# Optimization experiments

Measured on AMD Instinct MI355X. Metric: run time of the kernel, lower is better.

Reference implementation:

```python
import jax, jax.numpy as jnp
import numpy as np
from jax import lax

D_MODEL = 1024
INTER = 1024
N_EXPERTS = 8
TOP_K = 2
ROUTE_SCALE = 1.0
B, S = 2, 4096


def setup_inputs() -> dict:
    key = jax.random.key(0)
    ks = jax.random.split(key, 16)
    sc_d = 1.0 / np.sqrt(D_MODEL)
    sc_f = 1.0 / np.sqrt(INTER)
    inp = {
        "x": jax.random.normal(ks[0], (B, S, D_MODEL), dtype=jnp.float32),
        "gate_w": jax.random.normal(ks[1], (N_EXPERTS, D_MODEL), dtype=jnp.float32) * sc_d,
        # stacked routed-expert SwiGLU params
        "w1": jax.random.normal(ks[2], (N_EXPERTS, D_MODEL, INTER), dtype=jnp.float32) * sc_d,
        "b1": jnp.zeros((N_EXPERTS, INTER), dtype=jnp.float32),
        "w2": jax.random.normal(ks[3], (N_EXPERTS, INTER, D_MODEL), dtype=jnp.float32) * sc_f,
        "b2": jnp.zeros((N_EXPERTS, D_MODEL), dtype=jnp.float32),
        "w3": jax.random.normal(ks[4], (N_EXPERTS, D_MODEL, INTER), dtype=jnp.float32) * sc_d,
        "b3": jnp.zeros((N_EXPERTS, INTER), dtype=jnp.float32),
        # shared expert (dense MLP on all tokens)
        "sw1": jax.random.normal(ks[5], (D_MODEL, INTER), dtype=jnp.float32) * sc_d,
        "sb1": jnp.zeros((INTER,), dtype=jnp.float32),
        "sw2": jax.random.normal(ks[6], (INTER, D_MODEL), dtype=jnp.float32) * sc_f,
        "sb2": jnp.zeros((D_MODEL,), dtype=jnp.float32),
        "sw3": jax.random.normal(ks[7], (D_MODEL, INTER), dtype=jnp.float32) * sc_d,
        "sb3": jnp.zeros((INTER,), dtype=jnp.float32),
    }
    return inp


def reference(x, gate_w, w1, b1, w2, b2, w3, b3, sw1, sb1, sw2, sb2, sw3, sb3):
    Bx, Sx, D = x.shape
    xt = x.reshape(-1, D)  # [T, D]

    # --- Gate: softmax scores, top-k experts (n_groups==1, no bias branch) ---
    scores = jax.nn.softmax((xt @ gate_w.T).astype(jnp.float32), axis=-1)  # [T, E]
    top_vals, top_idx = lax.top_k(scores, TOP_K)  # [T, K]
    weights = (top_vals * ROUTE_SCALE).astype(x.dtype)  # gather of original scores == top_vals

    # combine[t, e] = sum_k weights[t, k] * (top_idx[t, k] == e)
    combine = jnp.sum(
        jax.nn.one_hot(top_idx, N_EXPERTS, dtype=x.dtype) * weights[..., None], axis=1
    )  # [T, E]

    # --- Routed experts: scan over experts, weighted accumulate ---
    def body(acc, p):
        W1, B1, W2, B2, W3, B3, c = p  # c: [T] combine weights for this expert
        h = jax.nn.silu(xt @ W1 + B1) * (xt @ W3 + B3)  # [T, INTER]
        return acc + c[:, None] * (h @ W2 + B2), None

    y, _ = lax.scan(body, jnp.zeros_like(xt), (w1, b1, w2, b2, w3, b3, combine.T))

    # --- Shared expert on all tokens ---
    z = (jax.nn.silu(xt @ sw1 + sb1) * (xt @ sw3 + sb3)) @ sw2 + sb2

    return (y + z).reshape(Bx, Sx, D)
```

## Files before the change

### kernel.cpp

```cpp
#include <hip/hip_runtime.h>
#include <hip/hip_bf16.h>
#include <math.h>

#define D_MODEL 1024
#define INTER   1024
#define NEXP    8
#define T_TOK   8192
#define ROWCAP  17408

typedef short  short8 __attribute__((ext_vector_type(8)));
typedef float  f32x4  __attribute__((ext_vector_type(4)));

__device__ __forceinline__ ushort f2bf(float f) {
    uint u = __float_as_uint(f);
    u += 0x7fffu + ((u >> 16) & 1u);
    return (ushort)(u >> 16);
}
__device__ __forceinline__ float bf2f(ushort u) {
    return __uint_as_float((uint)u << 16);
}
__device__ __forceinline__ uint pk2(float lo, float hi) {
    return (uint)f2bf(lo) | ((uint)f2bf(hi) << 16);
}
__device__ __forceinline__ void gll16(const ushort* g, ushort* l) {
    __builtin_amdgcn_global_load_lds(
        (const __attribute__((address_space(1))) unsigned int*)(g),
        (__attribute__((address_space(3))) unsigned int*)(l), 16, 0, 0);
}

#define IDX64(r, c) ((r) * 64 + (((c) ^ ((r) & 7)) * 8))

__global__ __launch_bounds__(256)
void k_gate(const float* __restrict__ X, const float* __restrict__ GW,
            int* __restrict__ topk_idx, float* __restrict__ topk_w,
            int* __restrict__ cnt, ushort* __restrict__ Xb)
{
    __shared__ int lcnt[NEXP];
    const int t = threadIdx.x;
    if (t < NEXP) lcnt[t] = 0;
    const int lane = t & 63, wv = t >> 6;
    float4 gwr[NEXP][4];
#pragma unroll
    for (int e = 0; e < NEXP; ++e)
#pragma unroll
        for (int i = 0; i < 4; ++i)
            gwr[e][i] = *(const float4*)(GW + e * 1024 + i * 256 + lane * 4);
    __syncthreads();
    const int tok0 = blockIdx.x * 32 + wv * 8;
    const bool b0 = lane & 1, b1 = lane & 2, b2 = lane & 4;
    for (int tt = 0; tt < 8; ++tt) {
        const int tok = tok0 + tt;
        const float* xr = X + (size_t)tok * 1024;
        float4 xv[4];
#pragma unroll
        for (int i = 0; i < 4; ++i) xv[i] = *(const float4*)(xr + i * 256 + lane * 4);
#pragma unroll
        for (int i = 0; i < 4; ++i) {
            uint2 o = { pk2(xv[i].x, xv[i].y), pk2(xv[i].z, xv[i].w) };
            *(uint2*)(Xb + (size_t)tok * 1024 + i * 256 + lane * 4) = o;
        }
        float p[NEXP];
#pragma unroll
        for (int e = 0; e < NEXP; ++e) {
            float s = 0.f;
#pragma unroll
            for (int i = 0; i < 4; ++i)
                s += xv[i].x * gwr[e][i].x + xv[i].y * gwr[e][i].y
                   + xv[i].z * gwr[e][i].z + xv[i].w * gwr[e][i].w;
            p[e] = s;
        }
        float q[4];
#pragma unroll
        for (int j = 0; j < 4; ++j) {
            float send = b0 ? p[j] : p[j + 4];
            float recv = __shfl_xor(send, 1, 64);
            q[j] = (b0 ? p[j + 4] : p[j]) + recv;
        }
        float u2[2];
#pragma unroll
        for (int j = 0; j < 2; ++j) {
            float send = b1 ? q[j] : q[j + 2];
            float recv = __shfl_xor(send, 2, 64);
            u2[j] = (b1 ? q[j + 2] : q[j]) + recv;
        }
        float send = b2 ? u2[0] : u2[1];
        float r = (b2 ? u2[1] : u2[0]) + __shfl_xor(send, 4, 64);
        r += __shfl_xor(r, 8, 64);
        r += __shfl_xor(r, 16, 64);
        r += __shfl_xor(r, 32, 64);
        float sc[NEXP];
#pragma unroll
        for (int e = 0; e < NEXP; ++e)
            sc[e] = __shfl(r, ((e & 1) << 2) | (e & 2) | ((e >> 2) & 1), 64);
        float m = sc[0];
#pragma unroll
        for (int e = 1; e < NEXP; ++e) m = fmaxf(m, sc[e]);
        float ssum = 0.f;
#pragma unroll
        for (int e = 0; e < NEXP; ++e) { sc[e] = __expf(sc[e] - m); ssum += sc[e]; }
        float inv = 1.f / ssum;
#pragma unroll
        for (int e = 0; e < NEXP; ++e) sc[e] *= inv;
        int i0 = 0; float v0 = sc[0];
#pragma unroll
        for (int e = 1; e < NEXP; ++e) if (sc[e] > v0) { v0 = sc[e]; i0 = e; }
        int i1 = -1; float v1 = -1e30f;
#pragma unroll
        for (int e = 0; e < NEXP; ++e) if (e != i0 && sc[e] > v1) { v1 = sc[e]; i1 = e; }
        if (lane == 0) {
            topk_idx[2 * tok]     = i0;
            topk_idx[2 * tok + 1] = i1;
            topk_w[2 * tok]       = v0;
            topk_w[2 * tok + 1]   = v1;
            atomicAdd(&lcnt[i0], 1);
            atomicAdd(&lcnt[i1], 1);
        }
    }
    __syncthreads();
    if (t < NEXP) atomicAdd(&cnt[t], lcnt[t]);
}

__global__ void k_prefix(const int* __restrict__ cnt, int* __restrict__ offs)
{
    if (threadIdx.x == 0 && blockIdx.x == 0) {
        int tot = 0;
        for (int e = 0; e < NEXP; ++e) {
            offs[e] = tot;
            tot += ((cnt[e] + 127) / 128) * 128;
        }
        offs[NEXP] = tot;
    }
}

__global__ void k_scatter(const int* __restrict__ topk_idx, const float* __restrict__ topk_w,
                          const int* __restrict__ offs, int* __restrict__ cnt2,
                          int* __restrict__ rowid, float* __restrict__ rowwt,
                          int* __restrict__ rowslot)
{
    __shared__ int loc[NEXP];
    __shared__ int base[NEXP];
    const int t = threadIdx.x;
    if (t < NEXP) loc[t] = 0;
    __syncthreads();
    const int tok = blockIdx.x * 256 + t;
    const int e0 = topk_idx[2 * tok], e1 = topk_idx[2 * tok + 1];
    const int s0 = atomicAdd(&loc[e0], 1);
    const int s1 = atomicAdd(&loc[e1], 1);
    __syncthreads();
    if (t < NEXP) base[t] = atomicAdd(&cnt2[t], loc[t]);
    __syncthreads();
    int p0 = offs[e0] + base[e0] + s0;
    rowid[p0] = tok; rowwt[p0] = topk_w[2 * tok]; rowslot[p0] = 0;
    int p1 = offs[e1] + base[e1] + s1;
    rowid[p1] = tok; rowwt[p1] = topk_w[2 * tok + 1]; rowslot[p1] = 1;
}

__global__ __launch_bounds__(256)
void k_tw(const float* __restrict__ srcA, ushort* __restrict__ dstA, int nA,
          const float* __restrict__ srcB, ushort* __restrict__ dstB, int nB,
          const float* __restrict__ srcC, ushort* __restrict__ dstC)
{
    __shared__ float tl[64][132];
    int m = blockIdx.y;
    const float* src; ushort* dst;
    if (m < nA)           { src = srcA + ((size_t)m << 20); dst = dstA + ((size_t)m << 20); }
    else if ((m -= nA) < nB) { src = srcB + ((size_t)m << 20); dst = dstB + ((size_t)m << 20); }
    else { m -= nB;       src = srcC + ((size_t)m << 20); dst = dstC + ((size_t)m << 20); }
    const int tile = blockIdx.x;
    const int nb = tile >> 4, kt = tile & 15;
    const int t = threadIdx.x;
    const int c4 = (t & 31) * 4, kr = t >> 5;
#pragma unroll
    for (int i = 0; i < 8; ++i) {
        const int kl = kr + 8 * i;
        float4 v = *(const float4*)(src + (size_t)(kt * 64 + kl) * 1024 + nb * 128 + c4);
        tl[kl][c4 + 0] = v.x; tl[kl][c4 + 1] = v.y;
        tl[kl][c4 + 2] = v.z; tl[kl][c4 + 3] = v.w;
    }
    __syncthreads();
    const int nl = t >> 1, h = t & 1;
    ushort* drow = dst + (size_t)tile * 8192 + nl * 64;
#pragma unroll
    for (int w = 0; w < 4; ++w) {
        const int cimg = h * 4 + w;
        const int cl = cimg ^ (nl & 7);
        float f[8];
#pragma unroll
        for (int j = 0; j < 8; ++j) f[j] = tl[cl * 8 + j][nl];
        uint4 o = { pk2(f[0], f[1]), pk2(f[2], f[3]), pk2(f[4], f[5]), pk2(f[6], f[7]) };
        *(uint4*)(drow + cimg * 8) = o;
    }
}

template <bool ROUTED>
__global__ __launch_bounds__(256, 2)
void k_h(const ushort* __restrict__ Xb,
         const ushort* __restrict__ W1t, const float* __restrict__ B1,
         const ushort* __restrict__ W3t, const float* __restrict__ B3,
         ushort* __restrict__ Hb,
         const int* __restrict__ rowid, const int* __restrict__ offs,
         const int* __restrict__ cnt)
{
    __shared__ __align__(16) ushort As [128 * 64];
    __shared__ __align__(16) ushort B1s[128 * 64];
    __shared__ __align__(16) ushort B3s[128 * 64];
    __shared__ int ridc[128];

    const int bid = blockIdx.y * 8 + blockIdx.x;
    const int swz = (bid & 7) * gridDim.y + (bid >> 3);
    const int nbx  = swz & 7;
    const int nb   = nbx * 128;
    const int row0 = (swz >> 3) * 128;

    int rstart = 0, rcount = T_TOK;
    const ushort* w1 = W1t; const ushort* w3 = W3t;
    if constexpr (ROUTED) {
        const int total = offs[NEXP];
        if (row0 >= total) return;
        int e = 0;
        while (offs[e + 1] <= row0) ++e;
        rstart = offs[e]; rcount = cnt[e];
        w1 += (size_t)e << 20; B1 += e * INTER;
        w3 += (size_t)e << 20; B3 += e * INTER;
    }
    const int t = threadIdx.x;
    const ushort* g1 = w1 + (size_t)(nbx * 16) * 8192 + t * 8;
    const ushort* g3 = w3 + (size_t)(nbx * 16) * 8192 + t * 8;

    if constexpr (ROUTED) {
        if (t < 128) {
            const int rr = row0 + t;
            ridc[t] = ((rr - rstart) < rcount) ? rowid[rr] : 0;
        }
        __syncthreads();
    }
    const int sub = t >> 3, ci = t & 7;
    const ushort* asrc[4];
#pragma unroll
    for (int c = 0; c < 4; ++c) {
        const int r = c * 32 + sub;
        const int tok = ROUTED ? ridc[r] : (row0 + r);
        asrc[c] = Xb + (size_t)tok * 1024 + (size_t)((ci ^ (sub & 7)) * 8);
    }

    const int lane = t & 63, wid = t >> 6;
    const int wm = wid & 1, wn = wid >> 1;
    const int m16 = lane & 15, g = lane >> 4;
    int offA[2][4], offB[2][4];
#pragma unroll
    for (int ks = 0; ks < 2; ++ks)
#pragma unroll
        for (int i = 0; i < 4; ++i) {
            offA[ks][i] = IDX64(wm * 64 + i * 16 + m16, ks * 4 + g);
            offB[ks][i] = IDX64(wn * 64 + i * 16 + m16, ks * 4 + g);
        }

    const f32x4 zf = {0.f, 0.f, 0.f, 0.f};
    f32x4 acc1[4][4], acc3[4][4];
#pragma unroll
    for (int i = 0; i < 4; ++i)
#pragma unroll
        for (int j = 0; j < 4; ++j) { acc1[i][j] = zf; acc3[i][j] = zf; }

    for (int kt = 0; kt < 16; ++kt) {
        __syncthreads();
#pragma unroll
        for (int c = 0; c < 4; ++c)
            gll16(asrc[c] + kt * 64, &As[c * 2048 + t * 8]);
#pragma unroll
        for (int c = 0; c < 4; ++c) {
            gll16(g1 + kt * 8192 + c * 2048, &B1s[c * 2048 + t * 8]);
            gll16(g3 + kt * 8192 + c * 2048, &B3s[c * 2048 + t * 8]);
        }
        __syncthreads();
#pragma unroll
        for (int ks = 0; ks < 2; ++ks) {
            short8 af[4], b1f[4], b3f[4];
#pragma unroll
            for (int i = 0; i < 4; ++i) {
                af[i]  = *(const short8*)&As [offA[ks][i]];
                b1f[i] = *(const short8*)&B1s[offB[ks][i]];
                b3f[i] = *(const short8*)&B3s[offB[ks][i]];
            }
#pragma unroll
            for (int i = 0; i < 4; ++i)
#pragma unroll
                for (int j = 0; j < 4; ++j) {
                    acc1[i][j] = __builtin_amdgcn_mfma_f32_16x16x32_bf16(af[i], b1f[j], acc1[i][j], 0, 0, 0);
                    acc3[i][j] = __builtin_amdgcn_mfma_f32_16x16x32_bf16(af[i], b3f[j], acc3[i][j], 0, 0, 0);
                }
        }
    }

#pragma unroll
    for (int j = 0; j < 4; ++j) {
        const int gcol = nb + wn * 64 + j * 16 + m16;
        const float bb1 = B1[gcol];
        const float bb3 = B3[gcol];
#pragma unroll
        for (int i = 0; i < 4; ++i) {
            const int growb = row0 + wm * 64 + i * 16 + g * 4;
#pragma unroll
            for (int r = 0; r < 4; ++r) {
                float x1 = acc1[i][j][r] + bb1;
                float x3 = acc3[i][j][r] + bb3;
                float h = x1 / (1.f + __expf(-x1)) * x3;
                Hb[(size_t)(growb + r) * INTER + gcol] = f2bf(h);
            }
        }
    }
}

template <int MODE>
__global__ __launch_bounds__(256, 2)
void k_out(const ushort* __restrict__ Hin,
           const ushort* __restrict__ W2t, const float* __restrict__ B2,
           float* __restrict__ out,
           const int* __restrict__ rowid, const int* __restrict__ offs,
           const int* __restrict__ cnt, const float* __restrict__ rowwt,
           const int* __restrict__ rowslot, ushort* __restrict__ Yb)
{
    __shared__ __align__(16) ushort As[128 * 64];
    __shared__ __align__(16) ushort Bs[128 * 64];

    const int bid = blockIdx.y * 8 + blockIdx.x;
    const int swz = (bid & 7) * gridDim.y + (bid >> 3);
    const int nbx  = swz & 7;
    const int nb   = nbx * 128;
    const int row0 = (swz >> 3) * 128;

    int rstart = 0, rcount = T_TOK;
    const ushort* w2 = W2t;
    if constexpr (MODE != 0) {
        const int total = offs[NEXP];
        if (row0 >= total) return;
        int e = 0;
        while (offs[e + 1] <= row0) ++e;
        rstart = offs[e]; rcount = cnt[e];
        w2 += (size_t)e << 20; B2 += e * D_MODEL;
    }
    const int t = threadIdx.x;
    const ushort* g2 = w2 + (size_t)(nbx * 16) * 8192 + t * 8;

    const int sub = t >> 3, ci = t & 7;
    const ushort* asrc[4];
#pragma unroll
    for (int c = 0; c < 4; ++c) {
        const int r = c * 32 + sub;
        asrc[c] = Hin + (size_t)(row0 + r) * 1024 + (size_t)((ci ^ (sub & 7)) * 8);
    }

    const int lane = t & 63, wid = t >> 6;
    const int wm = wid & 1, wn = wid >> 1;
    const int m16 = lane & 15, g = lane >> 4;
    int offA[2][4], offB[2][4];
#pragma unroll
    for (int ks = 0; ks < 2; ++ks)
#pragma unroll
        for (int i = 0; i < 4; ++i) {
            offA[ks][i] = IDX64(wm * 64 + i * 16 + m16, ks * 4 + g);
            offB[ks][i] = IDX64(wn * 64 + i * 16 + m16, ks * 4 + g);
        }

    const f32x4 zf = {0.f, 0.f, 0.f, 0.f};
    f32x4 acc[4][4];
#pragma unroll
    for (int i = 0; i < 4; ++i)
#pragma unroll
        for (int j = 0; j < 4; ++j) acc[i][j] = zf;

    for (int kt = 0; kt < 16; ++kt) {
        __syncthreads();
#pragma unroll
        for (int c = 0; c < 4; ++c)
            gll16(asrc[c] + kt * 64, &As[c * 2048 + t * 8]);
#pragma unroll
        for (int c = 0; c < 4; ++c)
            gll16(g2 + kt * 8192 + c * 2048, &Bs[c * 2048 + t * 8]);
        __syncthreads();
#pragma unroll
        for (int ks = 0; ks < 2; ++ks) {
            short8 af[4], bf[4];
#pragma unroll
            for (int i = 0; i < 4; ++i) {
                af[i] = *(const short8*)&As[offA[ks][i]];
                bf[i] = *(const short8*)&Bs[offB[ks][i]];
            }
#pragma unroll
            for (int i = 0; i < 4; ++i)
#pragma unroll
                for (int j = 0; j < 4; ++j)
                    acc[i][j] = __builtin_amdgcn_mfma_f32_16x16x32_bf16(af[i], bf[j], acc[i][j], 0, 0, 0);
        }
    }

#pragma unroll
    for (int i = 0; i < 4; ++i) {
#pragma unroll
        for (int r = 0; r < 4; ++r) {
            const int grow = row0 + wm * 64 + i * 16 + g * 4 + r;
            if constexpr (MODE == 0) {
#pragma unroll
                for (int j = 0; j < 4; ++j) {
                    const int gcol = nb + wn * 64 + j * 16 + m16;
                    out[(size_t)grow * D_MODEL + gcol] = acc[i][j][r] + B2[gcol];
                }
            } else {
                const bool valid = (grow - rstart) < rcount;
                if (!valid) continue;
                const int tok = rowid[grow];
                const float wt = rowwt[grow];
                const int sk = rowslot[grow];
                ushort* yr = Yb + (((size_t)sk * T_TOK + tok) << 10);
#pragma unroll
                for (int j = 0; j < 4; ++j) {
                    const int gcol = nb + wn * 64 + j * 16 + m16;
                    yr[gcol] = f2bf(wt * (acc[i][j][r] + B2[gcol]));
                }
            }
        }
    }
}

__global__ __launch_bounds__(256)
void k_combine(float* __restrict__ out, const ushort* __restrict__ Yb)
{
    const int row = blockIdx.x;
    const int c = threadIdx.x * 4;
    float4 o = *(const float4*)(out + (size_t)row * 1024 + c);
    ushort4 y0 = *(const ushort4*)(Yb + (size_t)row * 1024 + c);
    ushort4 y1 = *(const ushort4*)(Yb + ((size_t)(T_TOK + row)) * 1024 + c);
    o.x += bf2f(y0.x) + bf2f(y1.x);
    o.y += bf2f(y0.y) + bf2f(y1.y);
    o.z += bf2f(y0.z) + bf2f(y1.z);
    o.w += bf2f(y0.w) + bf2f(y1.w);
    *(float4*)(out + (size_t)row * 1024 + c) = o;
}

extern "C" void kernel_launch(void* const* d_in, const int* in_sizes, int n_in,
                              void* d_out, int out_size, void* d_ws, size_t ws_size,
                              hipStream_t stream)
{
    const float* x   = (const float*)d_in[0];
    const float* gw  = (const float*)d_in[1];
    const float* w1  = (const float*)d_in[2];
    const float* b1  = (const float*)d_in[3];
    const float* w2  = (const float*)d_in[4];
    const float* b2  = (const float*)d_in[5];
    const float* w3  = (const float*)d_in[6];
    const float* b3  = (const float*)d_in[7];
    const float* sw1 = (const float*)d_in[8];
    const float* sb1 = (const float*)d_in[9];
    const float* sw2 = (const float*)d_in[10];
    const float* sb2 = (const float*)d_in[11];
    const float* sw3 = (const float*)d_in[12];
    const float* sb3 = (const float*)d_in[13];
    float* out = (float*)d_out;

    char* ws = (char*)d_ws;
    int*   cnt      = (int*)(ws);
    int*   cnt2     = (int*)(ws + 64);
    int*   offs     = (int*)(ws + 128);
    int*   topk_idx = (int*)(ws + 256);
    float* topk_w   = (float*)(ws + 256 + 65536);
    int*   rowid    = (int*)(ws + 256 + 131072);
    float* rowwt    = (float*)(ws + 256 + 131072 + ROWCAP * 4);
    int*   rowslot  = (int*)(ws + 256 + 131072 + ROWCAP * 8);
    ushort* Hb = (ushort*)(ws + 524288);
    ushort* WA = (ushort*)(ws + 524288 + (size_t)ROWCAP * 2048);
    ushort* WB = WA + (8u << 20);
    ushort* WC = WB + (8u << 20);

    ushort* sw1t = WB;
    ushort* sw3t = WB + (1 << 20);
    ushort* sw2t = WA;
    ushort* w1t  = WA;
    ushort* w3t  = WB;
    ushort* w2t  = WC;
    ushort* Xbf  = WC;
    ushort* Yb   = WA;

    hipMemsetAsync(ws, 0, 256, stream);

    k_gate<<<256, 256, 0, stream>>>(x, gw, topk_idx, topk_w, cnt, Xbf);
    k_prefix<<<1, 64, 0, stream>>>(cnt, offs);
    k_scatter<<<32, 256, 0, stream>>>(topk_idx, topk_w, offs, cnt2, rowid, rowwt, rowslot);

    k_tw<<<dim3(128, 3), 256, 0, stream>>>(sw1, sw1t, 1, sw3, sw3t, 1, sw2, sw2t);
    k_h<false><<<dim3(8, 64), 256, 0, stream>>>(Xbf, sw1t, sb1, sw3t, sb3, Hb,
                                                nullptr, nullptr, nullptr);
    k_out<0><<<dim3(8, 64), 256, 0, stream>>>(Hb, sw2t, sb2, out,
                                              nullptr, nullptr, nullptr, nullptr,
                                              nullptr, nullptr);

    k_tw<<<dim3(128, 16), 256, 0, stream>>>(w1, w1t, 8, w3, w3t, 8, nullptr, nullptr);
    k_h<true><<<dim3(8, ROWCAP / 128), 256, 0, stream>>>(Xbf, w1t, b1, w3t, b3, Hb,
                                                         rowid, offs, cnt);
    k_tw<<<dim3(128, 8), 256, 0, stream>>>(w2, w2t, 8, nullptr, nullptr, 0,
                                           nullptr, nullptr);
    k_out<2><<<dim3(8, ROWCAP / 128), 256, 0, stream>>>(Hb, w2t, b2, out,
                                                        rowid, offs, cnt, rowwt,
                                                        rowslot, Yb);
    k_combine<<<T_TOK, 256, 0, stream>>>(out, Yb);
}
```

Measured before the change: 426.5 us.

## Halve GEMM N-tile to 64 for more blocks and merge weight conversion launches

The k_h and k_out GEMM kernels now use 128x64 output tiles instead of 128x128, doubling the grid and lowering register and LDS use so occupancy can rise to 3 blocks per CU. The shared-expert weight conversions are folded into a single k_tw launch together with the routed w1/w3 conversion, and the shared-expert weight buffers move into spare space after Hb so they do not collide with the routed buffers. Smaller tiles mean the A tile is reloaded twice as often per output, which adds global traffic, in exchange for better load balance and latency hiding.

```diff
diff --git a/kernel.cpp b/kernel.cpp
--- a/kernel.cpp
+++ b/kernel.cpp
@@ -156,16 +156,20 @@
 }
 
 __global__ __launch_bounds__(256)
-void k_tw(const float* __restrict__ srcA, ushort* __restrict__ dstA, int nA,
-          const float* __restrict__ srcB, ushort* __restrict__ dstB, int nB,
-          const float* __restrict__ srcC, ushort* __restrict__ dstC)
+void k_tw(const float* __restrict__ s1, ushort* __restrict__ d1, int n1,
+          const float* __restrict__ s2, ushort* __restrict__ d2, int n2,
+          const float* __restrict__ s3, ushort* __restrict__ d3, int n3,
+          const float* __restrict__ s4, ushort* __restrict__ d4, int n4,
+          const float* __restrict__ s5, ushort* __restrict__ d5)
 {
     __shared__ float tl[64][132];
     int m = blockIdx.y;
     const float* src; ushort* dst;
-    if (m < nA)           { src = srcA + ((size_t)m << 20); dst = dstA + ((size_t)m << 20); }
-    else if ((m -= nA) < nB) { src = srcB + ((size_t)m << 20); dst = dstB + ((size_t)m << 20); }
-    else { m -= nB;       src = srcC + ((size_t)m << 20); dst = dstC + ((size_t)m << 20); }
+    if (m < n1)              { src = s1 + ((size_t)m << 20); dst = d1 + ((size_t)m << 20); }
+    else if ((m -= n1) < n2) { src = s2 + ((size_t)m << 20); dst = d2 + ((size_t)m << 20); }
+    else if ((m -= n2) < n3) { src = s3 + ((size_t)m << 20); dst = d3 + ((size_t)m << 20); }
+    else if ((m -= n3) < n4) { src = s4 + ((size_t)m << 20); dst = d4 + ((size_t)m << 20); }
+    else { m -= n4;            src = s5 + ((size_t)m << 20); dst = d5 + ((size_t)m << 20); }
     const int tile = blockIdx.x;
     const int nb = tile >> 4, kt = tile & 15;
     const int t = threadIdx.x;
@@ -193,7 +197,7 @@
 }
 
 template <bool ROUTED>
-__global__ __launch_bounds__(256, 2)
+__global__ __launch_bounds__(256, 3)
 void k_h(const ushort* __restrict__ Xb,
          const ushort* __restrict__ W1t, const float* __restrict__ B1,
          const ushort* __restrict__ W3t, const float* __restrict__ B3,
@@ -202,15 +206,14 @@
          const int* __restrict__ cnt)
 {
     __shared__ __align__(16) ushort As [128 * 64];
-    __shared__ __align__(16) ushort B1s[128 * 64];
-    __shared__ __align__(16) ushort B3s[128 * 64];
+    __shared__ __align__(16) ushort B1s[64 * 64];
+    __shared__ __align__(16) ushort B3s[64 * 64];
     __shared__ int ridc[128];
 
-    const int bid = blockIdx.y * 8 + blockIdx.x;
-    const int swz = (bid & 7) * gridDim.y + (bid >> 3);
-    const int nbx  = swz & 7;
-    const int nb   = nbx * 128;
-    const int row0 = (swz >> 3) * 128;
+    const int bid = blockIdx.y * 16 + blockIdx.x;
+    const int swz = (bid & 7) * (gridDim.y * 2) + (bid >> 3);
+    const int nbx  = swz & 15;
+    const int row0 = (swz >> 4) * 128;
 
     int rstart = 0, rcount = T_TOK;
     const ushort* w1 = W1t; const ushort* w3 = W3t;
@@ -224,8 +227,8 @@
         w3 += (size_t)e << 20; B3 += e * INTER;
     }
     const int t = threadIdx.x;
-    const ushort* g1 = w1 + (size_t)(nbx * 16) * 8192 + t * 8;
-    const ushort* g3 = w3 + (size_t)(nbx * 16) * 8192 + t * 8;
+    const ushort* g1 = w1 + (size_t)(nbx >> 1) * 131072 + (nbx & 1) * 4096 + t * 8;
+    const ushort* g3 = w3 + (size_t)(nbx >> 1) * 131072 + (nbx & 1) * 4096 + t * 8;
 
     if constexpr (ROUTED) {
         if (t < 128) {
@@ -246,21 +249,23 @@
     const int lane = t & 63, wid = t >> 6;
     const int wm = wid & 1, wn = wid >> 1;
     const int m16 = lane & 15, g = lane >> 4;
-    int offA[2][4], offB[2][4];
-#pragma unroll
-    for (int ks = 0; ks < 2; ++ks)
-#pragma unroll
-        for (int i = 0; i < 4; ++i) {
+    int offA[2][4], offB[2][2];
+#pragma unroll
+    for (int ks = 0; ks < 2; ++ks) {
+#pragma unroll
+        for (int i = 0; i < 4; ++i)
             offA[ks][i] = IDX64(wm * 64 + i * 16 + m16, ks * 4 + g);
-            offB[ks][i] = IDX64(wn * 64 + i * 16 + m16, ks * 4 + g);
-        }
+#pragma unroll
+        for (int j = 0; j < 2; ++j)
+            offB[ks][j] = IDX64(wn * 32 + j * 16 + m16, ks * 4 + g);
+    }
 
     const f32x4 zf = {0.f, 0.f, 0.f, 0.f};
-    f32x4 acc1[4][4], acc3[4][4];
+    f32x4 acc1[4][2], acc3[4][2];
 #pragma unroll
     for (int i = 0; i < 4; ++i)
 #pragma unroll
-        for (int j = 0; j < 4; ++j) { acc1[i][j] = zf; acc3[i][j] = zf; }
+        for (int j = 0; j < 2; ++j) { acc1[i][j] = zf; acc3[i][j] = zf; }
 
     for (int kt = 0; kt < 16; ++kt) {
         __syncthreads();
@@ -268,24 +273,25 @@
         for (int c = 0; c < 4; ++c)
             gll16(asrc[c] + kt * 64, &As[c * 2048 + t * 8]);
 #pragma unroll
-        for (int c = 0; c < 4; ++c) {
-            gll16(g1 + kt * 8192 + c * 2048, &B1s[c * 2048 + t * 8]);
-            gll16(g3 + kt * 8192 + c * 2048, &B3s[c * 2048 + t * 8]);
+        for (int c = 0; c < 2; ++c) {
+            gll16(g1 + (size_t)kt * 8192 + c * 2048, &B1s[c * 2048 + t * 8]);
+            gll16(g3 + (size_t)kt * 8192 + c * 2048, &B3s[c * 2048 + t * 8]);
         }
         __syncthreads();
 #pragma unroll
         for (int ks = 0; ks < 2; ++ks) {
-            short8 af[4], b1f[4], b3f[4];
-#pragma unroll
-            for (int i = 0; i < 4; ++i) {
-                af[i]  = *(const short8*)&As [offA[ks][i]];
-                b1f[i] = *(const short8*)&B1s[offB[ks][i]];
-                b3f[i] = *(const short8*)&B3s[offB[ks][i]];
+            short8 af[4], b1f[2], b3f[2];
+#pragma unroll
+            for (int i = 0; i < 4; ++i) af[i] = *(const short8*)&As[offA[ks][i]];
+#pragma unroll
+            for (int j = 0; j < 2; ++j) {
+                b1f[j] = *(const short8*)&B1s[offB[ks][j]];
+                b3f[j] = *(const short8*)&B3s[offB[ks][j]];
             }
 #pragma unroll
             for (int i = 0; i < 4; ++i)
 #pragma unroll
-                for (int j = 0; j < 4; ++j) {
+                for (int j = 0; j < 2; ++j) {
                     acc1[i][j] = __builtin_amdgcn_mfma_f32_16x16x32_bf16(af[i], b1f[j], acc1[i][j], 0, 0, 0);
                     acc3[i][j] = __builtin_amdgcn_mfma_f32_16x16x32_bf16(af[i], b3f[j], acc3[i][j], 0, 0, 0);
                 }
@@ -293,8 +299,8 @@
     }
 
 #pragma unroll
-    for (int j = 0; j < 4; ++j) {
-        const int gcol = nb + wn * 64 + j * 16 + m16;
+    for (int j = 0; j < 2; ++j) {
+        const int gcol = nbx * 64 + wn * 32 + j * 16 + m16;
         const float bb1 = B1[gcol];
         const float bb3 = B3[gcol];
 #pragma unroll
@@ -312,7 +318,7 @@
 }
 
 template <int MODE>
-__global__ __launch_bounds__(256, 2)
+__global__ __launch_bounds__(256, 3)
 void k_out(const ushort* __restrict__ Hin,
            const ushort* __restrict__ W2t, const float* __restrict__ B2,
            float* __restrict__ out,
@@ -321,13 +327,12 @@
            const int* __restrict__ rowslot, ushort* __restrict__ Yb)
 {
     __shared__ __align__(16) ushort As[128 * 64];
-    __shared__ __align__(16) ushort Bs[128 * 64];
-
-    const int bid = blockIdx.y * 8 + blockIdx.x;
-    const int swz = (bid & 7) * gridDim.y + (bid >> 3);
-    const int nbx  = swz & 7;
-    const int nb   = nbx * 128;
-    const int row0 = (swz >> 3) * 128;
+    __shared__ __align__(16) ushort Bs[64 * 64];
+
+    const int bid = blockIdx.y * 16 + blockIdx.x;
+    const int swz = (bid & 7) * (gridDim.y * 2) + (bid >> 3);
+    const int nbx  = swz & 15;
+    const int row0 = (swz >> 4) * 128;
 
     int rstart = 0, rcount = T_TOK;
     const ushort* w2 = W2t;
@@ -340,7 +345,7 @@
         w2 += (size_t)e << 20; B2 += e * D_MODEL;
     }
     const int t = threadIdx.x;
-    const ushort* g2 = w2 + (size_t)(nbx * 16) * 8192 + t * 8;
+    const ushort* g2 = w2 + (size_t)(nbx >> 1) * 131072 + (nbx & 1) * 4096 + t * 8;
 
     const int sub = t >> 3, ci = t & 7;
     const ushort* asrc[4];
@@ -353,21 +358,23 @@
     const int lane = t & 63, wid = t >> 6;
     const int wm = wid & 1, wn = wid >> 1;
     const int m16 = lane & 15, g = lane >> 4;
-    int offA[2][4], offB[2][4];
-#pragma unroll
-    for (int ks = 0; ks < 2; ++ks)
-#pragma unroll
-        for (int i = 0; i < 4; ++i) {
+    int offA[2][4], offB[2][2];
+#pragma unroll
+    for (int ks = 0; ks < 2; ++ks) {
+#pragma unroll
+        for (int i = 0; i < 4; ++i)
             offA[ks][i] = IDX64(wm * 64 + i * 16 + m16, ks * 4 + g);
-            offB[ks][i] = IDX64(wn * 64 + i * 16 + m16, ks * 4 + g);
-        }
+#pragma unroll
+        for (int j = 0; j < 2; ++j)
+            offB[ks][j] = IDX64(wn * 32 + j * 16 + m16, ks * 4 + g);
+    }
 
     const f32x4 zf = {0.f, 0.f, 0.f, 0.f};
-    f32x4 acc[4][4];
+    f32x4 acc[4][2];
 #pragma unroll
     for (int i = 0; i < 4; ++i)
 #pragma unroll
-        for (int j = 0; j < 4; ++j) acc[i][j] = zf;
+        for (int j = 0; j < 2; ++j) acc[i][j] = zf;
 
     for (int kt = 0; kt < 16; ++kt) {
         __syncthreads();
@@ -375,21 +382,20 @@
         for (int c = 0; c < 4; ++c)
             gll16(asrc[c] + kt * 64, &As[c * 2048 + t * 8]);
 #pragma unroll
-        for (int c = 0; c < 4; ++c)
-            gll16(g2 + kt * 8192 + c * 2048, &Bs[c * 2048 + t * 8]);
+        for (int c = 0; c < 2; ++c)
+            gll16(g2 + (size_t)kt * 8192 + c * 2048, &Bs[c * 2048 + t * 8]);
         __syncthreads();
 #pragma unroll
         for (int ks = 0; ks < 2; ++ks) {
-            short8 af[4], bf[4];
-#pragma unroll
-            for (int i = 0; i < 4; ++i) {
-                af[i] = *(const short8*)&As[offA[ks][i]];
-                bf[i] = *(const short8*)&Bs[offB[ks][i]];
-            }
+            short8 af[4], bf[2];
+#pragma unroll
+            for (int i = 0; i < 4; ++i) af[i] = *(const short8*)&As[offA[ks][i]];
+#pragma unroll
+            for (int j = 0; j < 2; ++j) bf[j] = *(const short8*)&Bs[offB[ks][j]];
 #pragma unroll
             for (int i = 0; i < 4; ++i)
 #pragma unroll
-                for (int j = 0; j < 4; ++j)
+                for (int j = 0; j < 2; ++j)
                     acc[i][j] = __builtin_amdgcn_mfma_f32_16x16x32_bf16(af[i], bf[j], acc[i][j], 0, 0, 0);
         }
     }
@@ -401,8 +407,8 @@
             const int grow = row0 + wm * 64 + i * 16 + g * 4 + r;
             if constexpr (MODE == 0) {
 #pragma unroll
-                for (int j = 0; j < 4; ++j) {
-                    const int gcol = nb + wn * 64 + j * 16 + m16;
+                for (int j = 0; j < 2; ++j) {
+                    const int gcol = nbx * 64 + wn * 32 + j * 16 + m16;
                     out[(size_t)grow * D_MODEL + gcol] = acc[i][j][r] + B2[gcol];
                 }
             } else {
@@ -413,8 +419,8 @@
                 const int sk = rowslot[grow];
                 ushort* yr = Yb + (((size_t)sk * T_TOK + tok) << 10);
 #pragma unroll
-                for (int j = 0; j < 4; ++j) {
-                    const int gcol = nb + wn * 64 + j * 16 + m16;
+                for (int j = 0; j < 2; ++j) {
+                    const int gcol = nbx * 64 + wn * 32 + j * 16 + m16;
                     yr[gcol] = f2bf(wt * (acc[i][j][r] + B2[gcol]));
                 }
             }
@@ -471,9 +477,9 @@
     ushort* WB = WA + (8u << 20);
     ushort* WC = WB + (8u << 20);
 
-    ushort* sw1t = WB;
-    ushort* sw3t = WB + (1 << 20);
-    ushort* sw2t = WA;
+    ushort* sw1t = Hb + (8u << 20);
+    ushort* sw3t = sw1t + (1u << 20);
+    ushort* sw2t = sw3t + (1u << 20);
     ushort* w1t  = WA;
     ushort* w3t  = WB;
     ushort* w2t  = WC;
@@ -486,20 +492,23 @@
     k_prefix<<<1, 64, 0, stream>>>(cnt, offs);
     k_scatter<<<32, 256, 0, stream>>>(topk_idx, topk_w, offs, cnt2, rowid, rowwt, rowslot);
 
-    k_tw<<<dim3(128, 3), 256, 0, stream>>>(sw1, sw1t, 1, sw3, sw3t, 1, sw2, sw2t);
-    k_h<false><<<dim3(8, 64), 256, 0, stream>>>(Xbf, sw1t, sb1, sw3t, sb3, Hb,
-                                                nullptr, nullptr, nullptr);
-    k_out<0><<<dim3(8, 64), 256, 0, stream>>>(Hb, sw2t, sb2, out,
-                                              nullptr, nullptr, nullptr, nullptr,
-                                              nullptr, nullptr);
-
-    k_tw<<<dim3(128, 16), 256, 0, stream>>>(w1, w1t, 8, w3, w3t, 8, nullptr, nullptr);
-    k_h<true><<<dim3(8, ROWCAP / 128), 256, 0, stream>>>(Xbf, w1t, b1, w3t, b3, Hb,
-                                                         rowid, offs, cnt);
+    k_tw<<<dim3(128, 19), 256, 0, stream>>>(w1, w1t, 8, w3, w3t, 8,
+                                            sw1, sw1t, 1, sw3, sw3t, 1,
+                                            sw2, sw2t);
+
+    k_h<false><<<dim3(16, 64), 256, 0, stream>>>(Xbf, sw1t, sb1, sw3t, sb3, Hb,
+                                                 nullptr, nullptr, nullptr);
+    k_out<0><<<dim3(16, 64), 256, 0, stream>>>(Hb, sw2t, sb2, out,
+                                               nullptr, nullptr, nullptr, nullptr,
+                                               nullptr, nullptr);
+
+    k_h<true><<<dim3(16, ROWCAP / 128), 256, 0, stream>>>(Xbf, w1t, b1, w3t, b3, Hb,
+                                                          rowid, offs, cnt);
     k_tw<<<dim3(128, 8), 256, 0, stream>>>(w2, w2t, 8, nullptr, nullptr, 0,
+                                           nullptr, nullptr, 0, nullptr, nullptr, 0,
                                            nullptr, nullptr);
-    k_out<2><<<dim3(8, ROWCAP / 128), 256, 0, stream>>>(Hb, w2t, b2, out,
-                                                        rowid, offs, cnt, rowwt,
-                                                        rowslot, Yb);
+    k_out<2><<<dim3(16, ROWCAP / 128), 256, 0, stream>>>(Hb, w2t, b2, out,
+                                                         rowid, offs, cnt, rowwt,
+                                                         rowslot, Yb);
     k_combine<<<T_TOK, 256, 0, stream>>>(out, Yb);
 }
```

Result: faster. 414.9 us (-2.7%).
